# Kernel optimization log

Hardware: AMD Instinct MI355X
Metric: run time of the kernel (lower is better)

Reference implementation:

```python
import jax, jax.numpy as jnp
import numpy as np

FEATURE_DIM = 1024
N_CONCEPTS = 32768
BATCH = 1024
TEMPERATURE = 0.1
EPS = 1e-12  # matches torch F.normalize eps


def l2_normalize(x, axis=-1):
    n = jnp.linalg.norm(x, axis=axis, keepdims=True)
    return x / jnp.maximum(n, EPS)


def setup_inputs() -> dict:
    key = jax.random.key(0)
    k1, k2, k3, k4 = jax.random.split(key, 4)
    features = jax.random.normal(k1, (BATCH, FEATURE_DIM), dtype=jnp.float32)
    # Linear projection params (original inits to identity/zeros; random exercises the math)
    W = jnp.eye(FEATURE_DIM, dtype=jnp.float32) + 0.02 * jax.random.normal(k2, (FEATURE_DIM, FEATURE_DIM), dtype=jnp.float32)
    b = 0.01 * jax.random.normal(k3, (FEATURE_DIM,), dtype=jnp.float32)
    prototypes = l2_normalize(jax.random.normal(k4, (N_CONCEPTS, FEATURE_DIM), dtype=jnp.float32))
    return {"features": features, "W": W, "b": b, "prototypes": prototypes}


def reference(features, W, b, prototypes):
    # projection: features @ W.T + b   (torch nn.Linear convention)
    projected = jnp.einsum('bd,ed->be', features, W) + b          # [B, D]
    projected = l2_normalize(projected)                           # [B, D]
    # cosine similarity against all prototypes
    similarities = jnp.einsum('bd,kd->bk', projected, prototypes) # [B, K]
    activations = jax.nn.softmax(similarities / TEMPERATURE, axis=-1)
    best_idx = jnp.argmax(similarities, axis=-1)                  # [B] int
    return activations, best_idx
```

## Files before the change

### kernel.cpp

```cpp
#include <hip/hip_runtime.h>
#include <hip/hip_bf16.h>


typedef __attribute__((ext_vector_type(8))) short short8;
typedef __attribute__((ext_vector_type(4))) float floatx4;

__device__ __forceinline__ unsigned short f2bf(float f) {
  unsigned int u = __float_as_uint(f);
  u += 0x7fffu + ((u >> 16) & 1u);
  return (unsigned short)(u >> 16);
}
__device__ __forceinline__ float bf2f(unsigned short h) {
  return __uint_as_float(((unsigned int)h) << 16);
}

__global__ __launch_bounds__(256) void prep_convert(
    const float* __restrict__ protos, unsigned short* __restrict__ protoB,
    const float* __restrict__ features, unsigned short* __restrict__ Fh,
    unsigned short* __restrict__ Fm, unsigned short* __restrict__ Fl,
    const float* __restrict__ W, unsigned short* __restrict__ Wh,
    unsigned short* __restrict__ Wm, unsigned short* __restrict__ Wl) {
  const int blk = blockIdx.x;
  if (blk < 16384) {
    int i = blk * 256 + threadIdx.x;
    const float4* s4 = (const float4*)protos;
    float4 a = s4[2 * i];
    float4 b = s4[2 * i + 1];
    short8 o;
    o[0] = (short)f2bf(a.x); o[1] = (short)f2bf(a.y);
    o[2] = (short)f2bf(a.z); o[3] = (short)f2bf(a.w);
    o[4] = (short)f2bf(b.x); o[5] = (short)f2bf(b.y);
    o[6] = (short)f2bf(b.z); o[7] = (short)f2bf(b.w);
    ((short8*)protoB)[i] = o;
    return;
  }
  const float* src; unsigned short *H, *Md, *L; int i;
  if (blk < 17408) {
    src = features; H = Fh; Md = Fm; L = Fl;
    i = (blk - 16384) * 256 + threadIdx.x;
  } else {
    src = W; H = Wh; Md = Wm; L = Wl;
    i = (blk - 17408) * 256 + threadIdx.x;
  }
  float4 x = ((const float4*)src)[i];
  ushort4 h, m, l;
  float v, r;
  v = x.x; h.x = f2bf(v); r = v - bf2f(h.x); m.x = f2bf(r); l.x = f2bf(r - bf2f(m.x));
  v = x.y; h.y = f2bf(v); r = v - bf2f(h.y); m.y = f2bf(r); l.y = f2bf(r - bf2f(m.y));
  v = x.z; h.z = f2bf(v); r = v - bf2f(h.z); m.z = f2bf(r); l.z = f2bf(r - bf2f(m.z));
  v = x.w; h.w = f2bf(v); r = v - bf2f(h.w); m.w = f2bf(r); l.w = f2bf(r - bf2f(m.w));
  ((ushort4*)H)[i] = h; ((ushort4*)Md)[i] = m; ((ushort4*)L)[i] = l;
}


#define BARRIER() asm volatile("s_barrier" ::: "memory")
#define WAITLGKM()                                        \
  do {                                                    \
    asm volatile("s_waitcnt lgkmcnt(0)" ::: "memory");    \
    __builtin_amdgcn_sched_barrier(0);                    \
  } while (0)
#define WAITVM4() asm volatile("s_waitcnt vmcnt(4)" ::: "memory")

#define STAGE(OP, SLOT, H, KT)                                                 \
  do {                                                                         \
    const unsigned short* _s0 = (OP ? pB0 : pA0) + (H)*131072 + (KT)*64;       \
    const unsigned short* _s1 = (OP ? pB1 : pA1) + (H)*131072 + (KT)*64;       \
    __builtin_amdgcn_global_load_lds(                                          \
        (const __attribute__((address_space(1))) void*)_s0,                    \
        (__attribute__((address_space(3))) void*)(&lds[SLOT][OP][(H)*8192 + w * 512]), \
        16, 0, 0);                                                             \
    __builtin_amdgcn_global_load_lds(                                          \
        (const __attribute__((address_space(1))) void*)_s1,                    \
        (__attribute__((address_space(3))) void*)(&lds[SLOT][OP][(H)*8192 + 4096 + w * 512]), \
        16, 0, 0);                                                             \
  } while (0)

#define READ4(dst, base, off, rowadd)                                          \
  _Pragma("unroll") for (int q = 0; q < 4; q++)                                \
      dst[q] = *(const short8*)((base) + (off) + ((rowadd) + q) * 2048);

#define MFMA16(AB, BB, MBASE)                                                  \
  do {                                                                         \
    __builtin_amdgcn_sched_barrier(0);                                         \
    __builtin_amdgcn_s_setprio(1);                                             \
    _Pragma("unroll") for (int mf = 0; mf < 4; mf++)                           \
        _Pragma("unroll") for (int nf = 0; nf < 4; nf++)                       \
            acc[(MBASE) + mf][nf] = __builtin_amdgcn_mfma_f32_16x16x32_bf16(   \
                AB[mf], BB[nf], acc[(MBASE) + mf][nf], 0, 0, 0);               \
    __builtin_amdgcn_s_setprio(0);                                             \
    __builtin_amdgcn_sched_barrier(0);                                         \
  } while (0)

__global__ __launch_bounds__(512, 2) void gemm_nt_bf16_256(
    const unsigned short* __restrict__ A, const unsigned short* __restrict__ B,
    unsigned short* __restrict__ Cb, int M, int N, int K) {
  __shared__ unsigned short lds[2][2][16384];
  const int tid = threadIdx.x;
  const int w = tid >> 6, lane = tid & 63;
  const int wr = w >> 2, wc = w & 3;
  const int fr = lane & 15, koff8 = lane >> 4;

  const int bid = blockIdx.x;
  const int c8 = bid & 7, u = bid >> 3;
  const int nb = c8 * 16 + (u >> 2);
  const long tn = (long)nb * 256;
  const long tm = (long)(u & 3) * 256;

  const int idx0 = w * 64 + lane;
  const int idx1 = 512 + idx0;
  const int rh0 = idx0 >> 3, sc0 = (idx0 & 7) ^ (rh0 & 7);
  const int rh1 = idx1 >> 3, sc1 = (idx1 & 7) ^ (rh1 & 7);
  const unsigned short* pA0 = A + (tm + rh0) * 1024 + sc0 * 8;
  const unsigned short* pA1 = A + (tm + rh1) * 1024 + sc1 * 8;
  const unsigned short* pB0 = B + (tn + rh0) * 1024 + sc0 * 8;
  const unsigned short* pB1 = B + (tn + rh1) * 1024 + sc1 * 8;

  const int rA = wr * 128 + fr;
  const int rB = wc * 64 + fr;
  const int offA0 = rA * 128 + ((koff8 ^ (rA & 7)) << 4);
  const int offA1 = rA * 128 + (((koff8 ^ 4) ^ (rA & 7)) << 4);
  const int offB0 = rB * 128 + ((koff8 ^ (rB & 7)) << 4);
  const int offB1 = rB * 128 + (((koff8 ^ 4) ^ (rB & 7)) << 4);

  const char* ldsc = (const char*)&lds[0][0][0];
#define LDSA(s) (ldsc + (s)*65536)
#define LDSB(s) (ldsc + (s)*65536 + 32768)

  floatx4 acc[8][4];
#pragma unroll
  for (int i = 0; i < 8; i++)
#pragma unroll
    for (int j = 0; j < 4; j++) acc[i][j] = (floatx4){0.f, 0.f, 0.f, 0.f};

  short8 a0[4], a1[4], a2[4], b0[4], b1[4];

  STAGE(0, 0, 0, 0); STAGE(0, 0, 1, 0); STAGE(1, 0, 0, 0); STAGE(1, 0, 1, 0);
  STAGE(0, 1, 0, 1); STAGE(0, 1, 1, 1);
  WAITVM4();
  BARRIER();

#pragma unroll 1
  for (int i = 0; i < 8; i++) {
    const int t1 = 2 * i + 1;
    const int t2 = (2 * i + 2) & 15;
    const int t3 = (2 * i + 3) & 15;

    READ4(a0, LDSA(0), offA0, 0);
    READ4(a1, LDSA(0), offA0, 4);
    READ4(b0, LDSB(0), offB0, 0);
    STAGE(1, 1, 0, t1);
    BARRIER(); WAITLGKM();
    MFMA16(a0, b0, 0);
    BARRIER();
    READ4(a0, LDSA(0), offA1, 0);
    READ4(a2, LDSA(0), offA1, 4);
    READ4(b1, LDSB(0), offB1, 0);
    STAGE(1, 1, 1, t1);
    BARRIER(); WAITLGKM();
    MFMA16(a1, b0, 4);
    BARRIER();
    STAGE(0, 0, 0, t2);
    BARRIER();
    MFMA16(a0, b1, 0);
    BARRIER();
    STAGE(0, 0, 1, t2);
    WAITVM4();
    BARRIER();
    MFMA16(a2, b1, 4);
    BARRIER();

    READ4(a0, LDSA(1), offA0, 0);
    READ4(a1, LDSA(1), offA0, 4);
    READ4(b0, LDSB(1), offB0, 0);
    STAGE(1, 0, 0, t2);
    BARRIER(); WAITLGKM();
    MFMA16(a0, b0, 0);
    BARRIER();
    READ4(a0, LDSA(1), offA1, 0);
    READ4(a2, LDSA(1), offA1, 4);
    READ4(b1, LDSB(1), offB1, 0);
    STAGE(1, 0, 1, t2);
    BARRIER(); WAITLGKM();
    MFMA16(a1, b0, 4);
    BARRIER();
    STAGE(0, 1, 0, t3);
    BARRIER();
    MFMA16(a0, b1, 0);
    BARRIER();
    STAGE(0, 1, 1, t3);
    WAITVM4();
    BARRIER();
    MFMA16(a2, b1, 4);
    BARRIER();
  }

  const long crow = tm + wr * 128 + ((lane >> 4) * 4);
  const int cb = ((int)(tn >> 12)) * 8192;
  const int scol = ((int)tn & 4095) + wc * 64 + fr;
  const long rs2 = 2 * (long)N;
#pragma unroll
  for (int mf = 0; mf < 8; mf++)
#pragma unroll
    for (int nf = 0; nf < 4; nf++)
#pragma unroll
      for (int r = 0; r < 4; r++)
        Cb[(crow + mf * 16 + r) * rs2 + cb + scol + nf * 16] =
            f2bf(acc[mf][nf][r]);
#undef LDSA
#undef LDSB
}

__global__ __launch_bounds__(256) void gemm_split6_nt(
    const unsigned short* __restrict__ Ah, const unsigned short* __restrict__ Am,
    const unsigned short* __restrict__ Al, const unsigned short* __restrict__ Bh,
    const unsigned short* __restrict__ Bm, const unsigned short* __restrict__ Bl,
    float* __restrict__ Cpart, float* __restrict__ Cpart2, int M, int N, int K) {
  __shared__ unsigned short sA[3][64 * 32];
  __shared__ unsigned short sB[3][64 * 32];
  const int tid  = threadIdx.x;
  const int wave = tid >> 6;
  const int lane = tid & 63;
  const long tm = (long)blockIdx.y * 64;
  const long tn = (long)blockIdx.x * 64;
  const int wm = (wave & 1) * 32;
  const int wn = (wave >> 1) * 32;
  const int ksize = K / gridDim.z;
  const int kbase = blockIdx.z * ksize;
  float* C = (blockIdx.z < 2) ? (Cpart + (size_t)blockIdx.z * M * N)
                              : (Cpart2 + (size_t)(blockIdx.z - 2) * M * N);

  floatx4 accH[2][2], accL[2][2];
#pragma unroll
  for (int i = 0; i < 2; i++)
#pragma unroll
    for (int j = 0; j < 2; j++) {
      accH[i][j] = (floatx4){0.f, 0.f, 0.f, 0.f};
      accL[i][j] = (floatx4){0.f, 0.f, 0.f, 0.f};
    }

  const int rstage = tid >> 2;
  const int cstage = (tid & 3) * 8;
  const long aoff = (tm + rstage) * (long)K + cstage;
  const long boff = (tn + rstage) * (long)K + cstage;
  const unsigned short* Asrc[3] = {Ah + aoff, Am + aoff, Al + aoff};
  const unsigned short* Bsrc[3] = {Bh + boff, Bm + boff, Bl + boff};

  for (int k0 = kbase; k0 < kbase + ksize; k0 += 32) {
#pragma unroll
    for (int p = 0; p < 3; p++) {
      __builtin_amdgcn_global_load_lds(
          (const __attribute__((address_space(1))) void*)(Asrc[p] + k0),
          (__attribute__((address_space(3))) void*)(sA[p] + wave * 512), 16, 0, 0);
      __builtin_amdgcn_global_load_lds(
          (const __attribute__((address_space(1))) void*)(Bsrc[p] + k0),
          (__attribute__((address_space(3))) void*)(sB[p] + wave * 512), 16, 0, 0);
    }
    __syncthreads();

    const int fr = lane & 15;
    const int koff = (lane >> 4) * 8;
    short8 a_[3][2], b_[3][2];
#pragma unroll
    for (int p = 0; p < 3; p++)
#pragma unroll
      for (int mf = 0; mf < 2; mf++) {
        a_[p][mf] = *(const short8*)(sA[p] + (wm + mf * 16 + fr) * 32 + koff);
        b_[p][mf] = *(const short8*)(sB[p] + (wn + mf * 16 + fr) * 32 + koff);
      }
#pragma unroll
    for (int mf = 0; mf < 2; mf++)
#pragma unroll
      for (int nf = 0; nf < 2; nf++) {
        accH[mf][nf] = __builtin_amdgcn_mfma_f32_16x16x32_bf16(
            a_[0][mf], b_[0][nf], accH[mf][nf], 0, 0, 0);
        accL[mf][nf] = __builtin_amdgcn_mfma_f32_16x16x32_bf16(
            a_[0][mf], b_[1][nf], accL[mf][nf], 0, 0, 0);
        accL[mf][nf] = __builtin_amdgcn_mfma_f32_16x16x32_bf16(
            a_[1][mf], b_[0][nf], accL[mf][nf], 0, 0, 0);
        accL[mf][nf] = __builtin_amdgcn_mfma_f32_16x16x32_bf16(
            a_[0][mf], b_[2][nf], accL[mf][nf], 0, 0, 0);
        accL[mf][nf] = __builtin_amdgcn_mfma_f32_16x16x32_bf16(
            a_[2][mf], b_[0][nf], accL[mf][nf], 0, 0, 0);
        accL[mf][nf] = __builtin_amdgcn_mfma_f32_16x16x32_bf16(
            a_[1][mf], b_[1][nf], accL[mf][nf], 0, 0, 0);
      }
    __syncthreads();
  }

  const long crow = tm + wm + ((lane >> 4) * 4);
  const long ccol = tn + wn + (lane & 15);
#pragma unroll
  for (int mf = 0; mf < 2; mf++)
#pragma unroll
    for (int nf = 0; nf < 2; nf++)
#pragma unroll
      for (int r = 0; r < 4; r++)
        C[(crow + mf * 16 + r) * (long)N + ccol + nf * 16] =
            accH[mf][nf][r] + accL[mf][nf][r];
}

__global__ __launch_bounds__(256) void norm_bias_rows(
    const float* __restrict__ P0, const float* __restrict__ P1,
    const float* __restrict__ Q, int nparts,
    const float* __restrict__ bias, unsigned short* __restrict__ Pn,
    float* __restrict__ Pn32) {
  const int b = blockIdx.x, tid = threadIdx.x;
  const long ro = (long)b * 1024;
  float4 v = ((const float4*)(P0 + ro))[tid];
  if (nparts == 8) {
    float4 t;
    t = ((const float4*)(P1 + ro))[tid];
    v.x += t.x; v.y += t.y; v.z += t.z; v.w += t.w;
#pragma unroll
    for (int z = 0; z < 6; z++) {
      t = ((const float4*)(Q + (size_t)z * 1024 * 1024 + ro))[tid];
      v.x += t.x; v.y += t.y; v.z += t.z; v.w += t.w;
    }
  }
  float4 bb = ((const float4*)bias)[tid];
  v.x += bb.x; v.y += bb.y; v.z += bb.z; v.w += bb.w;
  float ss = v.x * v.x + v.y * v.y + v.z * v.z + v.w * v.w;
#pragma unroll
  for (int off = 32; off > 0; off >>= 1) ss += __shfl_down(ss, off);
  __shared__ float wred[4];
  if ((tid & 63) == 0) wred[tid >> 6] = ss;
  __syncthreads();
  float tot = wred[0] + wred[1] + wred[2] + wred[3];
  float inv = 1.0f / fmaxf(sqrtf(tot), 1e-12f);
  float4 p = make_float4(v.x * inv, v.y * inv, v.z * inv, v.w * inv);
  ((float4*)Pn32)[b * 256 + tid] = p;
  ushort4 o;
  o.x = f2bf(p.x); o.y = f2bf(p.y); o.z = f2bf(p.z); o.w = f2bf(p.w);
  ((ushort4*)Pn)[b * 256 + tid] = o;
}


__global__ __launch_bounds__(256) void row_ml_part(
    const float* __restrict__ out, float2* __restrict__ mlp,
    int* __restrict__ ncand) {
  const int bid = blockIdx.x;
  const int row = bid >> 3, chunk = bid & 7, tid = threadIdx.x;
  const int wave = tid >> 6, lane = tid & 63;
  if (chunk == 0 && tid == 0) ncand[row] = 0;
  const short8* src8 = (const short8*)((const char*)out +
                                       (size_t)row * 131072 +
                                       (size_t)chunk * 16384);
  short8 v0 = src8[tid];
  short8 v1 = src8[tid + 256];

  float z0 = bf2f((unsigned short)v0[0]) * 10.f;
  float z1 = bf2f((unsigned short)v0[1]) * 10.f;
  float z2 = bf2f((unsigned short)v0[2]) * 10.f;
  float z3 = bf2f((unsigned short)v0[3]) * 10.f;
  float z4 = bf2f((unsigned short)v0[4]) * 10.f;
  float z5 = bf2f((unsigned short)v0[5]) * 10.f;
  float z6 = bf2f((unsigned short)v0[6]) * 10.f;
  float z7 = bf2f((unsigned short)v0[7]) * 10.f;
  float y0 = bf2f((unsigned short)v1[0]) * 10.f;
  float y1 = bf2f((unsigned short)v1[1]) * 10.f;
  float y2 = bf2f((unsigned short)v1[2]) * 10.f;
  float y3 = bf2f((unsigned short)v1[3]) * 10.f;
  float y4 = bf2f((unsigned short)v1[4]) * 10.f;
  float y5 = bf2f((unsigned short)v1[5]) * 10.f;
  float y6 = bf2f((unsigned short)v1[6]) * 10.f;
  float y7 = bf2f((unsigned short)v1[7]) * 10.f;
  float m = fmaxf(
      fmaxf(fmaxf(fmaxf(z0, z1), fmaxf(z2, z3)), fmaxf(fmaxf(z4, z5), fmaxf(z6, z7))),
      fmaxf(fmaxf(fmaxf(y0, y1), fmaxf(y2, y3)), fmaxf(fmaxf(y4, y5), fmaxf(y6, y7))));
  float l = __expf(z0 - m) + __expf(z1 - m) + __expf(z2 - m) + __expf(z3 - m) +
            __expf(z4 - m) + __expf(z5 - m) + __expf(z6 - m) + __expf(z7 - m) +
            __expf(y0 - m) + __expf(y1 - m) + __expf(y2 - m) + __expf(y3 - m) +
            __expf(y4 - m) + __expf(y5 - m) + __expf(y6 - m) + __expf(y7 - m);
#pragma unroll
  for (int off = 1; off < 64; off <<= 1) {
    float mo = __shfl_xor(m, off);
    float lo = __shfl_xor(l, off);
    float nm = fmaxf(m, mo);
    l = l * __expf(m - nm) + lo * __expf(mo - nm);
    m = nm;
  }
  __shared__ float sm_[4], sl_[4];
  if (lane == 0) { sm_[wave] = m; sl_[wave] = l; }
  __syncthreads();
  if (tid == 0) {
    float Mb = fmaxf(fmaxf(sm_[0], sm_[1]), fmaxf(sm_[2], sm_[3]));
    float Lb = sl_[0] * __expf(sm_[0] - Mb) + sl_[1] * __expf(sm_[1] - Mb) +
               sl_[2] * __expf(sm_[2] - Mb) + sl_[3] * __expf(sm_[3] - Mb);
    mlp[bid] = make_float2(Mb, Lb);
  }
}

__global__ __launch_bounds__(256) void act_cand(
    float* __restrict__ out, const float2* __restrict__ mlp,
    int* __restrict__ ncand, int* __restrict__ candlist) {
  const int bid = blockIdx.x;
  const int row = bid >> 3, chunk = bid & 7, tid = threadIdx.x;

  float2 q0 = mlp[row * 8 + 0], q1 = mlp[row * 8 + 1];
  float2 q2 = mlp[row * 8 + 2], q3 = mlp[row * 8 + 3];
  float2 q4 = mlp[row * 8 + 4], q5 = mlp[row * 8 + 5];
  float2 q6 = mlp[row * 8 + 6], q7 = mlp[row * 8 + 7];
  const float Mz = fmaxf(fmaxf(fmaxf(q0.x, q1.x), fmaxf(q2.x, q3.x)),
                         fmaxf(fmaxf(q4.x, q5.x), fmaxf(q6.x, q7.x)));
  const float L = q0.y * __expf(q0.x - Mz) + q1.y * __expf(q1.x - Mz) +
                  q2.y * __expf(q2.x - Mz) + q3.y * __expf(q3.x - Mz) +
                  q4.y * __expf(q4.x - Mz) + q5.y * __expf(q5.x - Mz) +
                  q6.y * __expf(q6.x - Mz) + q7.y * __expf(q7.x - Mz);
  const float invL = 1.0f / L;
  const float thr = Mz * 0.1f - 0.016f;

  const short8* src8 = (const short8*)((const char*)out +
                                       (size_t)row * 131072 +
                                       (size_t)chunk * 16384);
  short8 v0 = src8[tid];
  short8 v1 = src8[tid + 256];
  __syncthreads();

  float* orow = out + (long)row * 32768;
#pragma unroll
  for (int j = 0; j < 2; j++) {
    const int i8 = chunk * 512 + tid + 256 * j;
    short8 v = (j == 0) ? v0 : v1;
    float s0 = bf2f((unsigned short)v[0]);
    float s1 = bf2f((unsigned short)v[1]);
    float s2 = bf2f((unsigned short)v[2]);
    float s3 = bf2f((unsigned short)v[3]);
    float s4 = bf2f((unsigned short)v[4]);
    float s5 = bf2f((unsigned short)v[5]);
    float s6 = bf2f((unsigned short)v[6]);
    float s7 = bf2f((unsigned short)v[7]);
    float mx = fmaxf(fmaxf(fmaxf(s0, s1), fmaxf(s2, s3)),
                     fmaxf(fmaxf(s4, s5), fmaxf(s6, s7)));
    if (mx >= thr) {
      if (s0 >= thr) { int p = atomicAdd(&ncand[row], 1); if (p < 64) candlist[row * 64 + p] = i8 * 8 + 0; }
      if (s1 >= thr) { int p = atomicAdd(&ncand[row], 1); if (p < 64) candlist[row * 64 + p] = i8 * 8 + 1; }
      if (s2 >= thr) { int p = atomicAdd(&ncand[row], 1); if (p < 64) candlist[row * 64 + p] = i8 * 8 + 2; }
      if (s3 >= thr) { int p = atomicAdd(&ncand[row], 1); if (p < 64) candlist[row * 64 + p] = i8 * 8 + 3; }
      if (s4 >= thr) { int p = atomicAdd(&ncand[row], 1); if (p < 64) candlist[row * 64 + p] = i8 * 8 + 4; }
      if (s5 >= thr) { int p = atomicAdd(&ncand[row], 1); if (p < 64) candlist[row * 64 + p] = i8 * 8 + 5; }
      if (s6 >= thr) { int p = atomicAdd(&ncand[row], 1); if (p < 64) candlist[row * 64 + p] = i8 * 8 + 6; }
      if (s7 >= thr) { int p = atomicAdd(&ncand[row], 1); if (p < 64) candlist[row * 64 + p] = i8 * 8 + 7; }
    }
    float4 e0, e1;
    e0.x = __expf(s0 * 10.f - Mz) * invL;
    e0.y = __expf(s1 * 10.f - Mz) * invL;
    e0.z = __expf(s2 * 10.f - Mz) * invL;
    e0.w = __expf(s3 * 10.f - Mz) * invL;
    e1.x = __expf(s4 * 10.f - Mz) * invL;
    e1.y = __expf(s5 * 10.f - Mz) * invL;
    e1.z = __expf(s6 * 10.f - Mz) * invL;
    e1.w = __expf(s7 * 10.f - Mz) * invL;
    ((float4*)orow)[2 * i8] = e0;
    ((float4*)orow)[2 * i8 + 1] = e1;
  }
}

__global__ __launch_bounds__(256) void argmax_refine(
    const int* __restrict__ ncand, const int* __restrict__ candlist,
    const float* __restrict__ Pn32, const float* __restrict__ protos,
    float* __restrict__ idx_out) {
  const int b = blockIdx.x, tid = threadIdx.x;
  const int wave = tid >> 6, lane = tid & 63;
  int n = ncand[b]; n = n < 64 ? n : 64;
  float4 pv = ((const float4*)(Pn32 + (long)b * 1024))[tid];
  __shared__ double dred[4];
  double best = -1e300;
  int besti = 0x7fffffff;
  for (int c = 0; c < n; c++) {
    int k = candlist[b * 64 + c];
    float4 kv = ((const float4*)(protos + (long)k * 1024))[tid];
    double d = (double)pv.x * kv.x + (double)pv.y * kv.y +
               (double)pv.z * kv.z + (double)pv.w * kv.w;
#pragma unroll
    for (int off = 32; off > 0; off >>= 1) d += __shfl_down(d, off);
    if (lane == 0) dred[wave] = d;
    __syncthreads();
    if (tid == 0) {
      double tot = dred[0] + dred[1] + dred[2] + dred[3];
      if (tot > best || (tot == best && k < besti)) { best = tot; besti = k; }
    }
    __syncthreads();
  }
  if (tid == 0) idx_out[b] = (float)besti;
}

extern "C" void kernel_launch(void* const* d_in, const int* in_sizes, int n_in,
                              void* d_out, int out_size, void* d_ws, size_t ws_size,
                              hipStream_t stream) {
  const float* features = (const float*)d_in[0];
  const float* W        = (const float*)d_in[1];
  const float* bias     = (const float*)d_in[2];
  const float* protos   = (const float*)d_in[3];

  const size_t MB = 1024 * 1024;
  char* ws = (char*)d_ws;
  unsigned short* protoB = (unsigned short*)ws;
  unsigned short* Fh = (unsigned short*)(ws + 64 * MB);
  unsigned short* Fm = (unsigned short*)(ws + 66 * MB);
  unsigned short* Fl = (unsigned short*)(ws + 68 * MB);
  unsigned short* Wh = (unsigned short*)(ws + 70 * MB);
  unsigned short* Wm = (unsigned short*)(ws + 72 * MB);
  unsigned short* Wl = (unsigned short*)(ws + 74 * MB);
  float*          P0 = (float*)(ws + 76 * MB);
  float*          P1 = (float*)(ws + 80 * MB);
  float*          Q  = (float*)d_out;
  unsigned short* Pn   = (unsigned short*)(ws + 64 * MB);
  float*          Pn32 = (float*)(ws + 66 * MB);
  float2* mlp      = (float2*)(ws + 70 * MB);
  int*    ncand    = (int*)(ws + 70 * MB + 128 * 1024);
  int*    candlist = (int*)(ws + 70 * MB + 256 * 1024);

  const int ksplit = (ws_size >= 84 * MB) ? 8 : 1;

  float* S = (float*)d_out;
  float* idx_out = S + (size_t)1024 * 32768;

  prep_convert<<<18432, 256, 0, stream>>>(protos, protoB, features, Fh, Fm, Fl,
                                          W, Wh, Wm, Wl);
  gemm_split6_nt<<<dim3(16, 16, ksplit), 256, 0, stream>>>(
      Fh, Fm, Fl, Wh, Wm, Wl, P0, Q, 1024, 1024, 1024);
  norm_bias_rows<<<1024, 256, 0, stream>>>(P0, P1, Q, ksplit, bias, Pn, Pn32);
  gemm_nt_bf16_256<<<512, 512, 0, stream>>>(Pn, protoB, (unsigned short*)d_out,
                                            1024, 32768, 1024);
  row_ml_part<<<8192, 256, 0, stream>>>(S, mlp, ncand);
  act_cand<<<8192, 256, 0, stream>>>(S, mlp, ncand, candlist);
  argmax_refine<<<1024, 256, 0, stream>>>(ncand, candlist, Pn32, protos,
                                          idx_out);
}
```

Baseline: 409.6 us.

## Fuse fp32-to-split-bf16 conversion into projection GEMM and merge with proto conversion

The projection GEMM now reads fp32 features and W directly and splits them into hi/mid/lo bf16 in registers before writing to LDS. This removes the separate split arrays and their global round trip. The GEMM blocks are appended to the prototype conversion launch, which drops one kernel launch. The K-split is reduced from 8 to 4, so the partial-sum reduction reads fewer buffers. The cost is redundant conversion work per tile, since each element is converted by 16 blocks. The loads also become synchronous register loads instead of async global-to-LDS copies.

```diff
diff --git a/kernel.cpp b/kernel.cpp
--- a/kernel.cpp
+++ b/kernel.cpp
@@ -14,15 +14,33 @@
   return __uint_as_float(((unsigned int)h) << 16);
 }
 
-__global__ __launch_bounds__(256) void prep_convert(
+__device__ __forceinline__ void split8(float4 x, float4 y, short8* h,
+                                       short8* m, short8* l) {
+  float vv[8] = {x.x, x.y, x.z, x.w, y.x, y.y, y.z, y.w};
+  short8 hh, mm, ll;
+#pragma unroll
+  for (int j = 0; j < 8; j++) {
+    float v = vv[j];
+    unsigned short hj = f2bf(v);
+    float r = v - bf2f(hj);
+    unsigned short mj = f2bf(r);
+    unsigned short lj = f2bf(r - bf2f(mj));
+    hh[j] = (short)hj; mm[j] = (short)mj; ll[j] = (short)lj;
+  }
+  *h = hh; *m = mm; *l = ll;
+}
+
+__global__ __launch_bounds__(256) void prep_proj(
     const float* __restrict__ protos, unsigned short* __restrict__ protoB,
-    const float* __restrict__ features, unsigned short* __restrict__ Fh,
-    unsigned short* __restrict__ Fm, unsigned short* __restrict__ Fl,
-    const float* __restrict__ W, unsigned short* __restrict__ Wh,
-    unsigned short* __restrict__ Wm, unsigned short* __restrict__ Wl) {
+    const float* __restrict__ F, const float* __restrict__ W,
+    float* __restrict__ Cpart, float* __restrict__ Cpart2, int nz) {
+  __shared__ unsigned short sA[3][2048];
+  __shared__ unsigned short sB[3][2048];
   const int blk = blockIdx.x;
+  const int tid = threadIdx.x;
+
   if (blk < 16384) {
-    int i = blk * 256 + threadIdx.x;
+    int i = blk * 256 + tid;
     const float4* s4 = (const float4*)protos;
     float4 a = s4[2 * i];
     float4 b = s4[2 * i + 1];
@@ -34,200 +52,18 @@
     ((short8*)protoB)[i] = o;
     return;
   }
-  const float* src; unsigned short *H, *Md, *L; int i;
-  if (blk < 17408) {
-    src = features; H = Fh; Md = Fm; L = Fl;
-    i = (blk - 16384) * 256 + threadIdx.x;
-  } else {
-    src = W; H = Wh; Md = Wm; L = Wl;
-    i = (blk - 17408) * 256 + threadIdx.x;
-  }
-  float4 x = ((const float4*)src)[i];
-  ushort4 h, m, l;
-  float v, r;
-  v = x.x; h.x = f2bf(v); r = v - bf2f(h.x); m.x = f2bf(r); l.x = f2bf(r - bf2f(m.x));
-  v = x.y; h.y = f2bf(v); r = v - bf2f(h.y); m.y = f2bf(r); l.y = f2bf(r - bf2f(m.y));
-  v = x.z; h.z = f2bf(v); r = v - bf2f(h.z); m.z = f2bf(r); l.z = f2bf(r - bf2f(m.z));
-  v = x.w; h.w = f2bf(v); r = v - bf2f(h.w); m.w = f2bf(r); l.w = f2bf(r - bf2f(m.w));
-  ((ushort4*)H)[i] = h; ((ushort4*)Md)[i] = m; ((ushort4*)L)[i] = l;
-}
-
-
-#define BARRIER() asm volatile("s_barrier" ::: "memory")
-#define WAITLGKM()                                        \
-  do {                                                    \
-    asm volatile("s_waitcnt lgkmcnt(0)" ::: "memory");    \
-    __builtin_amdgcn_sched_barrier(0);                    \
-  } while (0)
-#define WAITVM4() asm volatile("s_waitcnt vmcnt(4)" ::: "memory")
-
-#define STAGE(OP, SLOT, H, KT)                                                 \
-  do {                                                                         \
-    const unsigned short* _s0 = (OP ? pB0 : pA0) + (H)*131072 + (KT)*64;       \
-    const unsigned short* _s1 = (OP ? pB1 : pA1) + (H)*131072 + (KT)*64;       \
-    __builtin_amdgcn_global_load_lds(                                          \
-        (const __attribute__((address_space(1))) void*)_s0,                    \
-        (__attribute__((address_space(3))) void*)(&lds[SLOT][OP][(H)*8192 + w * 512]), \
-        16, 0, 0);                                                             \
-    __builtin_amdgcn_global_load_lds(                                          \
-        (const __attribute__((address_space(1))) void*)_s1,                    \
-        (__attribute__((address_space(3))) void*)(&lds[SLOT][OP][(H)*8192 + 4096 + w * 512]), \
-        16, 0, 0);                                                             \
-  } while (0)
-
-#define READ4(dst, base, off, rowadd)                                          \
-  _Pragma("unroll") for (int q = 0; q < 4; q++)                                \
-      dst[q] = *(const short8*)((base) + (off) + ((rowadd) + q) * 2048);
-
-#define MFMA16(AB, BB, MBASE)                                                  \
-  do {                                                                         \
-    __builtin_amdgcn_sched_barrier(0);                                         \
-    __builtin_amdgcn_s_setprio(1);                                             \
-    _Pragma("unroll") for (int mf = 0; mf < 4; mf++)                           \
-        _Pragma("unroll") for (int nf = 0; nf < 4; nf++)                       \
-            acc[(MBASE) + mf][nf] = __builtin_amdgcn_mfma_f32_16x16x32_bf16(   \
-                AB[mf], BB[nf], acc[(MBASE) + mf][nf], 0, 0, 0);               \
-    __builtin_amdgcn_s_setprio(0);                                             \
-    __builtin_amdgcn_sched_barrier(0);                                         \
-  } while (0)
-
-__global__ __launch_bounds__(512, 2) void gemm_nt_bf16_256(
-    const unsigned short* __restrict__ A, const unsigned short* __restrict__ B,
-    unsigned short* __restrict__ Cb, int M, int N, int K) {
-  __shared__ unsigned short lds[2][2][16384];
-  const int tid = threadIdx.x;
-  const int w = tid >> 6, lane = tid & 63;
-  const int wr = w >> 2, wc = w & 3;
-  const int fr = lane & 15, koff8 = lane >> 4;
-
-  const int bid = blockIdx.x;
-  const int c8 = bid & 7, u = bid >> 3;
-  const int nb = c8 * 16 + (u >> 2);
-  const long tn = (long)nb * 256;
-  const long tm = (long)(u & 3) * 256;
-
-  const int idx0 = w * 64 + lane;
-  const int idx1 = 512 + idx0;
-  const int rh0 = idx0 >> 3, sc0 = (idx0 & 7) ^ (rh0 & 7);
-  const int rh1 = idx1 >> 3, sc1 = (idx1 & 7) ^ (rh1 & 7);
-  const unsigned short* pA0 = A + (tm + rh0) * 1024 + sc0 * 8;
-  const unsigned short* pA1 = A + (tm + rh1) * 1024 + sc1 * 8;
-  const unsigned short* pB0 = B + (tn + rh0) * 1024 + sc0 * 8;
-  const unsigned short* pB1 = B + (tn + rh1) * 1024 + sc1 * 8;
-
-  const int rA = wr * 128 + fr;
-  const int rB = wc * 64 + fr;
-  const int offA0 = rA * 128 + ((koff8 ^ (rA & 7)) << 4);
-  const int offA1 = rA * 128 + (((koff8 ^ 4) ^ (rA & 7)) << 4);
-  const int offB0 = rB * 128 + ((koff8 ^ (rB & 7)) << 4);
-  const int offB1 = rB * 128 + (((koff8 ^ 4) ^ (rB & 7)) << 4);
-
-  const char* ldsc = (const char*)&lds[0][0][0];
-#define LDSA(s) (ldsc + (s)*65536)
-#define LDSB(s) (ldsc + (s)*65536 + 32768)
-
-  floatx4 acc[8][4];
-#pragma unroll
-  for (int i = 0; i < 8; i++)
-#pragma unroll
-    for (int j = 0; j < 4; j++) acc[i][j] = (floatx4){0.f, 0.f, 0.f, 0.f};
-
-  short8 a0[4], a1[4], a2[4], b0[4], b1[4];
-
-  STAGE(0, 0, 0, 0); STAGE(0, 0, 1, 0); STAGE(1, 0, 0, 0); STAGE(1, 0, 1, 0);
-  STAGE(0, 1, 0, 1); STAGE(0, 1, 1, 1);
-  WAITVM4();
-  BARRIER();
-
-#pragma unroll 1
-  for (int i = 0; i < 8; i++) {
-    const int t1 = 2 * i + 1;
-    const int t2 = (2 * i + 2) & 15;
-    const int t3 = (2 * i + 3) & 15;
-
-    READ4(a0, LDSA(0), offA0, 0);
-    READ4(a1, LDSA(0), offA0, 4);
-    READ4(b0, LDSB(0), offB0, 0);
-    STAGE(1, 1, 0, t1);
-    BARRIER(); WAITLGKM();
-    MFMA16(a0, b0, 0);
-    BARRIER();
-    READ4(a0, LDSA(0), offA1, 0);
-    READ4(a2, LDSA(0), offA1, 4);
-    READ4(b1, LDSB(0), offB1, 0);
-    STAGE(1, 1, 1, t1);
-    BARRIER(); WAITLGKM();
-    MFMA16(a1, b0, 4);
-    BARRIER();
-    STAGE(0, 0, 0, t2);
-    BARRIER();
-    MFMA16(a0, b1, 0);
-    BARRIER();
-    STAGE(0, 0, 1, t2);
-    WAITVM4();
-    BARRIER();
-    MFMA16(a2, b1, 4);
-    BARRIER();
-
-    READ4(a0, LDSA(1), offA0, 0);
-    READ4(a1, LDSA(1), offA0, 4);
-    READ4(b0, LDSB(1), offB0, 0);
-    STAGE(1, 0, 0, t2);
-    BARRIER(); WAITLGKM();
-    MFMA16(a0, b0, 0);
-    BARRIER();
-    READ4(a0, LDSA(1), offA1, 0);
-    READ4(a2, LDSA(1), offA1, 4);
-    READ4(b1, LDSB(1), offB1, 0);
-    STAGE(1, 0, 1, t2);
-    BARRIER(); WAITLGKM();
-    MFMA16(a1, b0, 4);
-    BARRIER();
-    STAGE(0, 1, 0, t3);
-    BARRIER();
-    MFMA16(a0, b1, 0);
-    BARRIER();
-    STAGE(0, 1, 1, t3);
-    WAITVM4();
-    BARRIER();
-    MFMA16(a2, b1, 4);
-    BARRIER();
-  }
-
-  const long crow = tm + wr * 128 + ((lane >> 4) * 4);
-  const int cb = ((int)(tn >> 12)) * 8192;
-  const int scol = ((int)tn & 4095) + wc * 64 + fr;
-  const long rs2 = 2 * (long)N;
-#pragma unroll
-  for (int mf = 0; mf < 8; mf++)
-#pragma unroll
-    for (int nf = 0; nf < 4; nf++)
-#pragma unroll
-      for (int r = 0; r < 4; r++)
-        Cb[(crow + mf * 16 + r) * rs2 + cb + scol + nf * 16] =
-            f2bf(acc[mf][nf][r]);
-#undef LDSA
-#undef LDSB
-}
-
-__global__ __launch_bounds__(256) void gemm_split6_nt(
-    const unsigned short* __restrict__ Ah, const unsigned short* __restrict__ Am,
-    const unsigned short* __restrict__ Al, const unsigned short* __restrict__ Bh,
-    const unsigned short* __restrict__ Bm, const unsigned short* __restrict__ Bl,
-    float* __restrict__ Cpart, float* __restrict__ Cpart2, int M, int N, int K) {
-  __shared__ unsigned short sA[3][64 * 32];
-  __shared__ unsigned short sB[3][64 * 32];
-  const int tid  = threadIdx.x;
-  const int wave = tid >> 6;
-  const int lane = tid & 63;
-  const long tm = (long)blockIdx.y * 64;
-  const long tn = (long)blockIdx.x * 64;
+
+  const int u  = blk - 16384;
+  const int bx = u & 15, by = (u >> 4) & 15, bz = u >> 8;
+  const int wave = tid >> 6, lane = tid & 63;
+  const long tm = (long)by * 64;
+  const long tn = (long)bx * 64;
   const int wm = (wave & 1) * 32;
   const int wn = (wave >> 1) * 32;
-  const int ksize = K / gridDim.z;
-  const int kbase = blockIdx.z * ksize;
-  float* C = (blockIdx.z < 2) ? (Cpart + (size_t)blockIdx.z * M * N)
-                              : (Cpart2 + (size_t)(blockIdx.z - 2) * M * N);
+  const int ksize = 1024 / nz;
+  const int kbase = bz * ksize;
+  float* C = (bz < 2) ? (Cpart + (size_t)bz * 1024 * 1024)
+                      : (Cpart2 + (size_t)(bz - 2) * 1024 * 1024);
 
   floatx4 accH[2][2], accL[2][2];
 #pragma unroll
@@ -238,23 +74,26 @@
       accL[i][j] = (floatx4){0.f, 0.f, 0.f, 0.f};
     }
 
-  const int rstage = tid >> 2;
-  const int cstage = (tid & 3) * 8;
-  const long aoff = (tm + rstage) * (long)K + cstage;
-  const long boff = (tn + rstage) * (long)K + cstage;
-  const unsigned short* Asrc[3] = {Ah + aoff, Am + aoff, Al + aoff};
-  const unsigned short* Bsrc[3] = {Bh + boff, Bm + boff, Bl + boff};
+  const int srow = tid >> 2;
+  const int sc8  = (tid & 3) * 8;
+  const float* fA = F + (tm + srow) * 1024 + sc8;
+  const float* fB = W + (tn + srow) * 1024 + sc8;
+  const int soff = srow * 32 + sc8;
 
   for (int k0 = kbase; k0 < kbase + ksize; k0 += 32) {
-#pragma unroll
-    for (int p = 0; p < 3; p++) {
-      __builtin_amdgcn_global_load_lds(
-          (const __attribute__((address_space(1))) void*)(Asrc[p] + k0),
-          (__attribute__((address_space(3))) void*)(sA[p] + wave * 512), 16, 0, 0);
-      __builtin_amdgcn_global_load_lds(
-          (const __attribute__((address_space(1))) void*)(Bsrc[p] + k0),
-          (__attribute__((address_space(3))) void*)(sB[p] + wave * 512), 16, 0, 0);
-    }
+    float4 a0 = *(const float4*)(fA + k0);
+    float4 a1 = *(const float4*)(fA + k0 + 4);
+    float4 b0 = *(const float4*)(fB + k0);
+    float4 b1 = *(const float4*)(fB + k0 + 4);
+    short8 h, m, l;
+    split8(a0, a1, &h, &m, &l);
+    *(short8*)(sA[0] + soff) = h;
+    *(short8*)(sA[1] + soff) = m;
+    *(short8*)(sA[2] + soff) = l;
+    split8(b0, b1, &h, &m, &l);
+    *(short8*)(sB[0] + soff) = h;
+    *(short8*)(sB[1] + soff) = m;
+    *(short8*)(sB[2] + soff) = l;
     __syncthreads();
 
     const int fr = lane & 15;
@@ -295,27 +134,181 @@
     for (int nf = 0; nf < 2; nf++)
 #pragma unroll
       for (int r = 0; r < 4; r++)
-        C[(crow + mf * 16 + r) * (long)N + ccol + nf * 16] =
+        C[(crow + mf * 16 + r) * 1024 + ccol + nf * 16] =
             accH[mf][nf][r] + accL[mf][nf][r];
+}
+
+
+#define BARRIER() asm volatile("s_barrier" ::: "memory")
+#define WAITLGKM()                                        \
+  do {                                                    \
+    asm volatile("s_waitcnt lgkmcnt(0)" ::: "memory");    \
+    __builtin_amdgcn_sched_barrier(0);                    \
+  } while (0)
+#define WAITVM4() asm volatile("s_waitcnt vmcnt(4)" ::: "memory")
+
+#define STAGE(OP, SLOT, H, KT)                                                 \
+  do {                                                                         \
+    const unsigned short* _s0 = (OP ? pB0 : pA0) + (H)*131072 + (KT)*64;       \
+    const unsigned short* _s1 = (OP ? pB1 : pA1) + (H)*131072 + (KT)*64;       \
+    __builtin_amdgcn_global_load_lds(                                          \
+        (const __attribute__((address_space(1))) void*)_s0,                    \
+        (__attribute__((address_space(3))) void*)(&lds[SLOT][OP][(H)*8192 + w * 512]), \
+        16, 0, 0);                                                             \
+    __builtin_amdgcn_global_load_lds(                                          \
+        (const __attribute__((address_space(1))) void*)_s1,                    \
+        (__attribute__((address_space(3))) void*)(&lds[SLOT][OP][(H)*8192 + 4096 + w * 512]), \
+        16, 0, 0);                                                             \
+  } while (0)
+
+#define READ4(dst, base, off, rowadd)                                          \
+  _Pragma("unroll") for (int q = 0; q < 4; q++)                                \
+      dst[q] = *(const short8*)((base) + (off) + ((rowadd) + q) * 2048);
+
+#define MFMA16(AB, BB, MBASE)                                                  \
+  do {                                                                         \
+    __builtin_amdgcn_sched_barrier(0);                                         \
+    __builtin_amdgcn_s_setprio(1);                                             \
+    _Pragma("unroll") for (int mf = 0; mf < 4; mf++)                           \
+        _Pragma("unroll") for (int nf = 0; nf < 4; nf++)                       \
+            acc[(MBASE) + mf][nf] = __builtin_amdgcn_mfma_f32_16x16x32_bf16(   \
+                AB[mf], BB[nf], acc[(MBASE) + mf][nf], 0, 0, 0);               \
+    __builtin_amdgcn_s_setprio(0);                                             \
+    __builtin_amdgcn_sched_barrier(0);                                         \
+  } while (0)
+
+__global__ __launch_bounds__(512, 2) void gemm_nt_bf16_256(
+    const unsigned short* __restrict__ A, const unsigned short* __restrict__ B,
+    unsigned short* __restrict__ Cb, int M, int N, int K) {
+  __shared__ unsigned short lds[2][2][16384];
+  const int tid = threadIdx.x;
+  const int w = tid >> 6, lane = tid & 63;
+  const int wr = w >> 2, wc = w & 3;
+  const int fr = lane & 15, koff8 = lane >> 4;
+
+  const int bid = blockIdx.x;
+  const int c8 = bid & 7, u = bid >> 3;
+  const int nb = c8 * 16 + (u >> 2);
+  const long tn = (long)nb * 256;
+  const long tm = (long)(u & 3) * 256;
+
+  const int idx0 = w * 64 + lane;
+  const int idx1 = 512 + idx0;
+  const int rh0 = idx0 >> 3, sc0 = (idx0 & 7) ^ (rh0 & 7);
+  const int rh1 = idx1 >> 3, sc1 = (idx1 & 7) ^ (rh1 & 7);
+  const unsigned short* pA0 = A + (tm + rh0) * 1024 + sc0 * 8;
+  const unsigned short* pA1 = A + (tm + rh1) * 1024 + sc1 * 8;
+  const unsigned short* pB0 = B + (tn + rh0) * 1024 + sc0 * 8;
+  const unsigned short* pB1 = B + (tn + rh1) * 1024 + sc1 * 8;
+
+  const int rA = wr * 128 + fr;
+  const int rB = wc * 64 + fr;
+  const int offA0 = rA * 128 + ((koff8 ^ (rA & 7)) << 4);
+  const int offA1 = rA * 128 + (((koff8 ^ 4) ^ (rA & 7)) << 4);
+  const int offB0 = rB * 128 + ((koff8 ^ (rB & 7)) << 4);
+  const int offB1 = rB * 128 + (((koff8 ^ 4) ^ (rB & 7)) << 4);
+
+  const char* ldsc = (const char*)&lds[0][0][0];
+#define LDSA(s) (ldsc + (s)*65536)
+#define LDSB(s) (ldsc + (s)*65536 + 32768)
+
+  floatx4 acc[8][4];
+#pragma unroll
+  for (int i = 0; i < 8; i++)
+#pragma unroll
+    for (int j = 0; j < 4; j++) acc[i][j] = (floatx4){0.f, 0.f, 0.f, 0.f};
+
+  short8 a0[4], a1[4], a2[4], b0[4], b1[4];
+
+  STAGE(0, 0, 0, 0); STAGE(0, 0, 1, 0); STAGE(1, 0, 0, 0); STAGE(1, 0, 1, 0);
+  STAGE(0, 1, 0, 1); STAGE(0, 1, 1, 1);
+  WAITVM4();
+  BARRIER();
+
+#pragma unroll 1
+  for (int i = 0; i < 8; i++) {
+    const int t1 = 2 * i + 1;
+    const int t2 = (2 * i + 2) & 15;
+    const int t3 = (2 * i + 3) & 15;
+
+    READ4(a0, LDSA(0), offA0, 0);
+    READ4(a1, LDSA(0), offA0, 4);
+    READ4(b0, LDSB(0), offB0, 0);
+    STAGE(1, 1, 0, t1);
+    BARRIER(); WAITLGKM();
+    MFMA16(a0, b0, 0);
+    BARRIER();
+    READ4(a0, LDSA(0), offA1, 0);
+    READ4(a2, LDSA(0), offA1, 4);
+    READ4(b1, LDSB(0), offB1, 0);
+    STAGE(1, 1, 1, t1);
+    BARRIER(); WAITLGKM();
+    MFMA16(a1, b0, 4);
+    BARRIER();
+    STAGE(0, 0, 0, t2);
+    BARRIER();
+    MFMA16(a0, b1, 0);
+    BARRIER();
+    STAGE(0, 0, 1, t2);
+    WAITVM4();
+    BARRIER();
+    MFMA16(a2, b1, 4);
+    BARRIER();
+
+    READ4(a0, LDSA(1), offA0, 0);
+    READ4(a1, LDSA(1), offA0, 4);
+    READ4(b0, LDSB(1), offB0, 0);
+    STAGE(1, 0, 0, t2);
+    BARRIER(); WAITLGKM();
+    MFMA16(a0, b0, 0);
+    BARRIER();
+    READ4(a0, LDSA(1), offA1, 0);
+    READ4(a2, LDSA(1), offA1, 4);
+    READ4(b1, LDSB(1), offB1, 0);
+    STAGE(1, 0, 1, t2);
+    BARRIER(); WAITLGKM();
+    MFMA16(a1, b0, 4);
+    BARRIER();
+    STAGE(0, 1, 0, t3);
+    BARRIER();
+    MFMA16(a0, b1, 0);
+    BARRIER();
+    STAGE(0, 1, 1, t3);
+    WAITVM4();
+    BARRIER();
+    MFMA16(a2, b1, 4);
+    BARRIER();
+  }
+
+  const long crow = tm + wr * 128 + ((lane >> 4) * 4);
+  const int cb = ((int)(tn >> 12)) * 8192;
+  const int scol = ((int)tn & 4095) + wc * 64 + fr;
+  const long rs2 = 2 * (long)N;
+#pragma unroll
+  for (int mf = 0; mf < 8; mf++)
+#pragma unroll
+    for (int nf = 0; nf < 4; nf++)
+#pragma unroll
+      for (int r = 0; r < 4; r++)
+        Cb[(crow + mf * 16 + r) * rs2 + cb + scol + nf * 16] =
+            f2bf(acc[mf][nf][r]);
+#undef LDSA
+#undef LDSB
 }
 
 __global__ __launch_bounds__(256) void norm_bias_rows(
     const float* __restrict__ P0, const float* __restrict__ P1,
-    const float* __restrict__ Q, int nparts,
+    const float* __restrict__ P2, const float* __restrict__ P3, int nparts,
     const float* __restrict__ bias, unsigned short* __restrict__ Pn,
     float* __restrict__ Pn32) {
   const int b = blockIdx.x, tid = threadIdx.x;
-  const long ro = (long)b * 1024;
-  float4 v = ((const float4*)(P0 + ro))[tid];
-  if (nparts == 8) {
-    float4 t;
-    t = ((const float4*)(P1 + ro))[tid];
-    v.x += t.x; v.y += t.y; v.z += t.z; v.w += t.w;
-#pragma unroll
-    for (int z = 0; z < 6; z++) {
-      t = ((const float4*)(Q + (size_t)z * 1024 * 1024 + ro))[tid];
-      v.x += t.x; v.y += t.y; v.z += t.z; v.w += t.w;
-    }
+  float4 v = ((const float4*)(P0 + (long)b * 1024))[tid];
+  if (nparts == 4) {
+    float4 v1 = ((const float4*)(P1 + (long)b * 1024))[tid];
+    float4 v2 = ((const float4*)(P2 + (long)b * 1024))[tid];
+    float4 v3 = ((const float4*)(P3 + (long)b * 1024))[tid];
+    v.x += v1.x + v2.x + v3.x; v.y += v1.y + v2.y + v3.y;
+    v.z += v1.z + v2.z + v3.z; v.w += v1.w + v2.w + v3.w;
   }
   float4 bb = ((const float4*)bias)[tid];
   v.x += bb.x; v.y += bb.y; v.z += bb.z; v.w += bb.w;
@@ -495,31 +488,25 @@
   const size_t MB = 1024 * 1024;
   char* ws = (char*)d_ws;
   unsigned short* protoB = (unsigned short*)ws;
-  unsigned short* Fh = (unsigned short*)(ws + 64 * MB);
-  unsigned short* Fm = (unsigned short*)(ws + 66 * MB);
-  unsigned short* Fl = (unsigned short*)(ws + 68 * MB);
-  unsigned short* Wh = (unsigned short*)(ws + 70 * MB);
-  unsigned short* Wm = (unsigned short*)(ws + 72 * MB);
-  unsigned short* Wl = (unsigned short*)(ws + 74 * MB);
-  float*          P0 = (float*)(ws + 76 * MB);
-  float*          P1 = (float*)(ws + 80 * MB);
-  float*          Q  = (float*)d_out;
   unsigned short* Pn   = (unsigned short*)(ws + 64 * MB);
   float*          Pn32 = (float*)(ws + 66 * MB);
   float2* mlp      = (float2*)(ws + 70 * MB);
   int*    ncand    = (int*)(ws + 70 * MB + 128 * 1024);
   int*    candlist = (int*)(ws + 70 * MB + 256 * 1024);
-
-  const int ksplit = (ws_size >= 84 * MB) ? 8 : 1;
+  float*          P0 = (float*)(ws + 76 * MB);
+  float*          P1 = (float*)(ws + 80 * MB);
+  float*          P2 = (float*)d_out;
+  float*          P3 = (float*)((char*)d_out + 4 * MB);
+
+  const int ksplit = (ws_size >= 84 * MB) ? 4 : 1;
 
   float* S = (float*)d_out;
   float* idx_out = S + (size_t)1024 * 32768;
 
-  prep_convert<<<18432, 256, 0, stream>>>(protos, protoB, features, Fh, Fm, Fl,
-                                          W, Wh, Wm, Wl);
-  gemm_split6_nt<<<dim3(16, 16, ksplit), 256, 0, stream>>>(
-      Fh, Fm, Fl, Wh, Wm, Wl, P0, Q, 1024, 1024, 1024);
-  norm_bias_rows<<<1024, 256, 0, stream>>>(P0, P1, Q, ksplit, bias, Pn, Pn32);
+  prep_proj<<<16384 + 256 * ksplit, 256, 0, stream>>>(
+      protos, protoB, features, W, P0, P2, ksplit);
+  norm_bias_rows<<<1024, 256, 0, stream>>>(P0, P1, P2, P3, ksplit, bias, Pn,
+                                           Pn32);
   gemm_nt_bf16_256<<<512, 512, 0, stream>>>(Pn, protoB, (unsigned short*)d_out,
                                             1024, 32768, 1024);
   row_ml_part<<<8192, 256, 0, stream>>>(S, mlp, ncand);
```

Measured after the change: 403.0 us. No clear change (-1.6%).
